# Optimization experiments

Hardware: AMD Instinct MI355X
Metric: run time of the kernel (lower is better)

## Reference

```python
import jax, jax.numpy as jnp
import numpy as np

NUM_SAMPLES = 100


def setup_inputs() -> dict:
    key = jax.random.key(0)
    # [B, 2C, H, W]: first C channels are logits, last C are log-std
    inp = jax.random.normal(key, (8, 38, 256, 256), dtype=jnp.float32)
    return {"input": inp}


def reference(input):
    logits, log_std = jnp.split(input, 2, axis=-3)  # each [B, C, H, W]
    std = jnp.exp(log_std)
    keys = jax.random.split(jax.random.key(1), NUM_SAMPLES)

    def body(acc, k):
        eps = jax.random.normal(k, std.shape, dtype=std.dtype)
        acc = acc + jax.nn.softmax(logits + eps * std, axis=-3)
        return acc, None

    softmax_sum, _ = jax.lax.scan(body, jnp.zeros_like(logits), keys)
    return softmax_sum / NUM_SAMPLES
```

## Files before the change

kernel.cpp:

```cpp
#include <hip/hip_runtime.h>
#include <stdint.h>


#define NCH    19
#define HW     65536
#define NSAMP  100

__device__ __forceinline__ uint32_t rotl(uint32_t x, uint32_t r) {
  return __builtin_amdgcn_alignbit(x, x, 32u - r);
}

__device__ __forceinline__ void tf2x32_full(uint32_t k0, uint32_t k1,
                                            uint32_t x0, uint32_t x1,
                                            uint32_t& o0, uint32_t& o1) {
  const uint32_t k2 = k0 ^ k1 ^ 0x1BD11BDAu;
#define TFR(r) { x0 += x1; x1 = rotl(x1, r) ^ x0; }
  x0 += k0; x1 += k1;
  TFR(13u) TFR(15u) TFR(26u) TFR(6u)
  x0 += k1; x1 += k2 + 1u;
  TFR(17u) TFR(29u) TFR(16u) TFR(24u)
  x0 += k2; x1 += k0 + 2u;
  TFR(13u) TFR(15u) TFR(26u) TFR(6u)
  x0 += k0; x1 += k1 + 3u;
  TFR(17u) TFR(29u) TFR(16u) TFR(24u)
  x0 += k1; x1 += k2 + 4u;
  TFR(13u) TFR(15u) TFR(26u) TFR(6u)
  x0 += k2; x1 += k0 + 5u;
#undef TFR
  o0 = x0; o1 = x1;
}

__device__ __forceinline__ uint32_t tf_fold(uint32_t k0, uint32_t k1, uint32_t k2,
                                            uint32_t x1in) {
  uint32_t x0, x1;
  x1 = x1in + k1;
  x0 = k0 + x1;
  x1 = rotl(x1, 13u) ^ x0;
  x0 += x1; x1 = rotl(x1, 15u) ^ x0;
  x0 += x1; x1 = rotl(x1, 26u) ^ x0;
  x0 += x1; x1 = rotl(x1,  6u) ^ x0;
  x1 += k2 + 1u;
  x0 = x0 + k1 + x1; x1 = rotl(x1, 17u) ^ x0;
  x0 += x1; x1 = rotl(x1, 29u) ^ x0;
  x0 += x1; x1 = rotl(x1, 16u) ^ x0;
  x0 += x1; x1 = rotl(x1, 24u) ^ x0;
  x1 += k0 + 2u;
  x0 = x0 + k2 + x1; x1 = rotl(x1, 13u) ^ x0;
  x0 += x1; x1 = rotl(x1, 15u) ^ x0;
  x0 += x1; x1 = rotl(x1, 26u) ^ x0;
  x0 += x1; x1 = rotl(x1,  6u) ^ x0;
  x1 += k1 + 3u;
  x0 = x0 + k0 + x1; x1 = rotl(x1, 17u) ^ x0;
  x0 += x1; x1 = rotl(x1, 29u) ^ x0;
  x0 += x1; x1 = rotl(x1, 16u) ^ x0;
  x0 += x1; x1 = rotl(x1, 24u) ^ x0;
  x1 += k2 + 4u;
  x0 = x0 + k1 + x1; x1 = rotl(x1, 13u) ^ x0;
  x0 += x1; x1 = rotl(x1, 15u) ^ x0;
  x0 += x1; x1 = rotl(x1, 26u) ^ x0;
  x0 += x1; x1 = rotl(x1,  6u) ^ x0;
  return (x0 + k2) ^ (x1 + k0 + 5u);
}

__device__ __forceinline__ float bits_to_eps(uint32_t bits) {
  const float lo = -0.99999994f;
  float f = __uint_as_float((bits >> 9) | 0x3F800000u) - 1.0f;
  float u = fmaf(f, 2.0f, lo);
  u = fmaxf(u, lo);
  float w = -__logf(fmaf(-u, u, 1.0f));
  float p;
  if (w < 5.0f) {
    w -= 2.5f;
    p = 3.9742683e-08f;
    p = fmaf(p, w, 4.8546493e-07f);
    p = fmaf(p, w, -4.9828230e-06f);
    p = fmaf(p, w, -6.2105302e-06f);
    p = fmaf(p, w, 3.0912002e-04f);
    p = fmaf(p, w, -1.7730354e-03f);
    p = fmaf(p, w, -5.9081371e-03f);
    p = fmaf(p, w, 3.4880267e-01f);
    p = fmaf(p, w, 2.1233141e+00f);
  } else {
    w = __fsqrt_rn(w) - 3.0f;
    p = -2.8314594e-04f;
    p = fmaf(p, w, 1.4276565e-04f);
    p = fmaf(p, w, 1.9082604e-03f);
    p = fmaf(p, w, -5.1950124e-03f);
    p = fmaf(p, w, 8.1168916e-03f);
    p = fmaf(p, w, -1.0779791e-02f);
    p = fmaf(p, w, 1.3348577e-02f);
    p = fmaf(p, w, 1.4165810e+00f);
    p = fmaf(p, w, 4.0064324e+00f);
  }
  return p * u;
}

__global__ __launch_bounds__(256, 2)
void HeteroscedasticSoftmax_kernel(const float* __restrict__ in,
                                   float* __restrict__ out) {
  __shared__ uint32_t sk0[NSAMP];
  __shared__ uint32_t sk1[NSAMP];
  const int t = threadIdx.x;
  if (t < NSAMP) {
    uint32_t a, b;
    tf2x32_full(0u, 1u, 0u, (uint32_t)t, a, b);
    sk0[t] = a;
    sk1[t] = b;
  }
  __syncthreads();

  const int gid = blockIdx.x * 256 + t;
  const int b_  = gid >> 16;
  const int hw  = gid & 65535;

  const float L2E = 1.4426950408889634f;
  const float* pin = in + (size_t)b_ * (2 * NCH * HW) + hw;
  float lgl[NCH], sdl[NCH], acc[NCH];
#pragma unroll
  for (int c = 0; c < NCH; ++c) {
    lgl[c] = pin[c * HW] * L2E;
    sdl[c] = __expf(pin[(NCH + c) * HW]) * L2E;
    acc[c] = 0.0f;
  }

  const uint32_t jbase = (uint32_t)(b_ * NCH) * (uint32_t)HW + (uint32_t)hw;

#pragma unroll 1
  for (int s = 0; s < NSAMP; ++s) {
    const uint32_t k0 = __builtin_amdgcn_readfirstlane(sk0[s]);
    const uint32_t k1 = __builtin_amdgcn_readfirstlane(sk1[s]);
    const uint32_t k2 = k0 ^ k1 ^ 0x1BD11BDAu;

    float z[NCH];
#pragma unroll
    for (int c = 0; c < NCH; ++c) {
      const uint32_t bits = tf_fold(k0, k1, k2, jbase + (uint32_t)c * HW);
      const float eps = bits_to_eps(bits);
      z[c] = fmaf(eps, sdl[c], lgl[c]);
    }

    float m0 = fmaxf(z[0], z[1]),  m1 = fmaxf(z[2], z[3]);
    float m2 = fmaxf(z[4], z[5]),  m3 = fmaxf(z[6], z[7]);
    float m4 = fmaxf(z[8], z[9]),  m5 = fmaxf(z[10], z[11]);
    float m6 = fmaxf(z[12], z[13]), m7 = fmaxf(z[14], z[15]);
    float m8 = fmaxf(z[16], z[17]);
    m0 = fmaxf(m0, m1); m2 = fmaxf(m2, m3); m4 = fmaxf(m4, m5);
    m6 = fmaxf(m6, m7); m8 = fmaxf(m8, z[18]);
    m0 = fmaxf(m0, m2); m4 = fmaxf(m4, m6);
    m0 = fmaxf(m0, m4);
    const float m = fmaxf(m0, m8);

#pragma unroll
    for (int c = 0; c < NCH; ++c) z[c] = __builtin_amdgcn_exp2f(z[c] - m);

    float s0 = z[0] + z[1],  s1 = z[2] + z[3];
    float s2 = z[4] + z[5],  s3 = z[6] + z[7];
    float s4 = z[8] + z[9],  s5 = z[10] + z[11];
    float s6 = z[12] + z[13], s7 = z[14] + z[15];
    float s8 = z[16] + z[17];
    s0 += s1; s2 += s3; s4 += s5; s6 += s7; s8 += z[18];
    s0 += s2; s4 += s6;
    s0 += s4;
    const float r = __builtin_amdgcn_rcpf(s0 + s8);

#pragma unroll
    for (int c = 0; c < NCH; ++c) acc[c] = fmaf(z[c], r, acc[c]);
  }

  float* pout = out + (size_t)b_ * (NCH * HW) + hw;
#pragma unroll
  for (int c = 0; c < NCH; ++c) pout[c * HW] = acc[c] * 0.01f;
}

extern "C" void kernel_launch(void* const* d_in, const int* in_sizes, int n_in,
                              void* d_out, int out_size, void* d_ws, size_t ws_size,
                              hipStream_t stream) {
  const float* in = (const float*)d_in[0];
  float* out = (float*)d_out;
  HeteroscedasticSoftmax_kernel<<<2048, 256, 0, stream>>>(in, out);
}
```

Measured before the change: 2.272 ms.

## Move per-pixel logits/std to LDS, raise occupancy, and simplify erfinv arithmetic

Per-channel scaled logits and std values now live in shared memory as float2 per thread instead of 38 registers, so launch bounds can request 4 waves per SIMD instead of 2. The erfinv polynomial is re-expressed in terms of log2 directly via the hardware log instruction, and the uniform mapping is folded into one fma, which removes a few scalar ops per sample. The cost is an LDS read for every channel and sample inside the hot loop, and the kernel now relies on the hardware log precision, which could slightly change the numerical results.

```diff
diff --git a/kernel.cpp b/kernel.cpp
--- a/kernel.cpp
+++ b/kernel.cpp
@@ -64,23 +64,24 @@
 
 __device__ __forceinline__ float bits_to_eps(uint32_t bits) {
   const float lo = -0.99999994f;
-  float f = __uint_as_float((bits >> 9) | 0x3F800000u) - 1.0f;
-  float u = fmaf(f, 2.0f, lo);
+  float x = __uint_as_float((bits >> 9) | 0x3F800000u);
+  float u = fmaf(x, 2.0f, -2.99999994f);
   u = fmaxf(u, lo);
-  float w = -__logf(fmaf(-u, u, 1.0f));
+  float t = __builtin_amdgcn_logf(fmaf(-u, u, 1.0f));
   float p;
-  if (w < 5.0f) {
-    w -= 2.5f;
-    p = 3.9742683e-08f;
-    p = fmaf(p, w, 4.8546493e-07f);
-    p = fmaf(p, w, -4.9828230e-06f);
-    p = fmaf(p, w, -6.2105302e-06f);
-    p = fmaf(p, w, 3.0912002e-04f);
-    p = fmaf(p, w, -1.7730354e-03f);
-    p = fmaf(p, w, -5.9081371e-03f);
-    p = fmaf(p, w, 3.4880267e-01f);
-    p = fmaf(p, w, 2.1233141e+00f);
+  if (t > -7.2135401f) {
+    float tw = t + 3.6067376f;
+    p = 2.1176667e-09f;
+    p = fmaf(p, tw, -3.7319753e-08f);
+    p = fmaf(p, tw, -5.5262077e-07f);
+    p = fmaf(p, tw, 9.9370361e-07f);
+    p = fmaf(p, tw, 7.1355918e-05f);
+    p = fmaf(p, tw, 5.9046852e-04f);
+    p = fmaf(p, tw, -2.8386612e-03f);
+    p = fmaf(p, tw, -2.4177230e-01f);
+    p = fmaf(p, tw, 2.1233141e+00f);
   } else {
+    float w = -0.69314718f * t;
     w = __fsqrt_rn(w) - 3.0f;
     p = -2.8314594e-04f;
     p = fmaf(p, w, 1.4276565e-04f);
@@ -95,19 +96,18 @@
   return p * u;
 }
 
-__global__ __launch_bounds__(256, 2)
+__global__ __launch_bounds__(256, 4)
 void HeteroscedasticSoftmax_kernel(const float* __restrict__ in,
                                    float* __restrict__ out) {
-  __shared__ uint32_t sk0[NSAMP];
-  __shared__ uint32_t sk1[NSAMP];
+  __shared__ float2 sls[NCH][256];
+  __shared__ uint2  skey[NSAMP];
+
   const int t = threadIdx.x;
   if (t < NSAMP) {
     uint32_t a, b;
     tf2x32_full(0u, 1u, 0u, (uint32_t)t, a, b);
-    sk0[t] = a;
-    sk1[t] = b;
+    skey[t] = make_uint2(a, b);
   }
-  __syncthreads();
 
   const int gid = blockIdx.x * 256 + t;
   const int b_  = gid >> 16;
@@ -115,20 +115,23 @@
 
   const float L2E = 1.4426950408889634f;
   const float* pin = in + (size_t)b_ * (2 * NCH * HW) + hw;
-  float lgl[NCH], sdl[NCH], acc[NCH];
+  float acc[NCH];
 #pragma unroll
   for (int c = 0; c < NCH; ++c) {
-    lgl[c] = pin[c * HW] * L2E;
-    sdl[c] = __expf(pin[(NCH + c) * HW]) * L2E;
+    float lg = pin[c * HW];
+    float ls = pin[(NCH + c) * HW];
+    sls[c][t] = make_float2(lg * L2E, __expf(ls) * L2E);
     acc[c] = 0.0f;
   }
+  __syncthreads();
 
   const uint32_t jbase = (uint32_t)(b_ * NCH) * (uint32_t)HW + (uint32_t)hw;
 
 #pragma unroll 1
   for (int s = 0; s < NSAMP; ++s) {
-    const uint32_t k0 = __builtin_amdgcn_readfirstlane(sk0[s]);
-    const uint32_t k1 = __builtin_amdgcn_readfirstlane(sk1[s]);
+    const uint2 kk = skey[s];
+    const uint32_t k0 = __builtin_amdgcn_readfirstlane(kk.x);
+    const uint32_t k1 = __builtin_amdgcn_readfirstlane(kk.y);
     const uint32_t k2 = k0 ^ k1 ^ 0x1BD11BDAu;
 
     float z[NCH];
@@ -136,7 +139,8 @@
     for (int c = 0; c < NCH; ++c) {
       const uint32_t bits = tf_fold(k0, k1, k2, jbase + (uint32_t)c * HW);
       const float eps = bits_to_eps(bits);
-      z[c] = fmaf(eps, sdl[c], lgl[c]);
+      const float2 ls = sls[c][t];
+      z[c] = fmaf(eps, ls.y, ls.x);
     }
 
     float m0 = fmaxf(z[0], z[1]),  m1 = fmaxf(z[2], z[3]);
```

Measured after the change: 2.119 ms. 6.7% less time.
